# Optimization experiments

Measured on AMD Instinct MI355X. Metric: run time of the kernel, lower is better.

## Reference

```python
import jax, jax.numpy as jnp
import numpy as np

N_NODES = 100000
N_EDGES = 3200000
HID = 32
N_LAYERS = 3
EDGE_DIM = 2
NODE_IN = 2          # [P, Q]
V_DIM = 2            # [V_mag, V_angle]
VH = V_DIM + HID     # 34, per-node feature fed to the GNN layer
MSG_IN = 2 * VH + EDGE_DIM   # 70
UPD_IN = VH + HID            # 66


def setup_inputs() -> dict:
    key = jax.random.key(0)
    ks = jax.random.split(key, 16)
    s = lambda *sh: 1.0 / np.sqrt(sh[-2]) if len(sh) >= 2 else 0.0
    inp = {
        "P_Q_inj": jax.random.normal(ks[0], (N_NODES, NODE_IN), dtype=jnp.float32),
        "senders": jax.random.randint(ks[1], (N_EDGES,), 0, N_NODES, dtype=jnp.int32),
        "receivers": jax.random.randint(ks[2], (N_EDGES,), 0, N_NODES, dtype=jnp.int32),
        "edge_features": jax.random.normal(ks[3], (N_EDGES, EDGE_DIM), dtype=jnp.float32),
        "edge_mask": jax.random.uniform(ks[4], (N_EDGES,), dtype=jnp.float32),
        # input embedding Dense(hidden_dim)
        "W_in": jax.random.normal(ks[5], (NODE_IN, HID), dtype=jnp.float32) * s(NODE_IN, HID),
        "b_in": jnp.zeros((HID,), dtype=jnp.float32),
        # per-layer params (flax compact loop -> distinct params per layer), stacked on axis 0
        "W_msg": jax.random.normal(ks[6], (N_LAYERS, MSG_IN, HID), dtype=jnp.float32) * s(MSG_IN, HID),
        "b_msg": jnp.zeros((N_LAYERS, HID), dtype=jnp.float32),
        "W_upd": jax.random.normal(ks[7], (N_LAYERS, UPD_IN, HID), dtype=jnp.float32) * s(UPD_IN, HID),
        "b_upd": jnp.zeros((N_LAYERS, HID), dtype=jnp.float32),
        "W_delta": jax.random.normal(ks[8], (N_LAYERS, HID, V_DIM), dtype=jnp.float32) * s(HID, V_DIM),
        "b_delta": jnp.zeros((N_LAYERS, V_DIM), dtype=jnp.float32),
    }
    return inp


def _layer(v, senders, receivers, edge_features, edge_mask, W_msg, b_msg, W_upd, b_upd):
    # v: [N, VH] node features. Gather sender/receiver feats, edge-wise MLP message,
    # soft mask, scatter-sum to receivers, then dense node update.
    msg_in = jnp.concatenate([v[senders], v[receivers], edge_features], axis=-1)  # [E, 70]
    m = jax.nn.relu(msg_in @ W_msg + b_msg)                                       # [E, H]
    m = m * edge_mask[:, None]
    agg = jax.ops.segment_sum(m, receivers, num_segments=v.shape[0])              # [N, H]
    v_out = jnp.concatenate([v, agg], axis=-1) @ W_upd + b_upd                    # [N, H]
    return v_out


def reference(P_Q_inj, senders, receivers, edge_features, edge_mask,
              W_in, b_in, W_msg, b_msg, W_upd, b_upd, W_delta, b_delta):
    V_pred = jnp.zeros_like(P_Q_inj).at[:, 0].set(1.0)   # [N, 2]
    h = P_Q_inj @ W_in + b_in                            # [N, H]
    for l in range(N_LAYERS):
        v_input = jnp.concatenate([V_pred, h], axis=-1)  # [N, 34]
        v_out = _layer(v_input, senders, receivers, edge_features, edge_mask,
                       W_msg[l], b_msg[l], W_upd[l], b_upd[l])
        h = jax.nn.relu(v_out)
        delta_V = h @ W_delta[l] + b_delta[l]
        V_pred = V_pred + delta_V
    return V_pred
```

## Files before the change

kernel.cpp:

```cpp
#include <hip/hip_runtime.h>
#include <hip/hip_fp16.h>

#define NN 100000
#define NE 3200000
#define NB 1563
#define NBLK ((NN + 255) / 256)
#define CHUNK 8192
#define NCH 391
#define CAP 4096

typedef float f32x4 __attribute__((ext_vector_type(4)));
typedef unsigned int u32x4 __attribute__((ext_vector_type(4)));

__device__ __forceinline__ float2 h2f2(unsigned int u) {
  __half2 h;
  *reinterpret_cast<unsigned int*>(&h) = u;
  return __half22float2(h);
}
__device__ __forceinline__ unsigned int f2h2(float x, float y) {
  __half2 h = __floats2half2_rn(x, y);
  return *reinterpret_cast<unsigned int*>(&h);
}


__global__ __launch_bounds__(256) void k_hist(const int* __restrict__ recv, int* __restrict__ histmat) {
  __shared__ int h[NB];
  int t = threadIdx.x, c = blockIdx.x;
  for (int i = t; i < NB; i += 256) h[i] = 0;
  __syncthreads();
  int start = c * CHUNK;
  int end = min(start + CHUNK, NE);
  for (int i = start + t; i < end; i += 256)
    atomicAdd(&h[__builtin_nontemporal_load(recv + i) >> 6], 1);
  __syncthreads();
  for (int i = t; i < NB; i += 256) histmat[i * NCH + c] = h[i];
}


__global__ __launch_bounds__(64) void k_scanA(const int* __restrict__ histmat, int* __restrict__ total) {
  __shared__ int ps[64];
  int t = threadIdx.x, b = blockIdx.x;
  int s = 0;
  for (int c = t; c < NCH; c += 64) s += histmat[b * NCH + c];
  ps[t] = s;
  __syncthreads();
  for (int o = 32; o > 0; o >>= 1) {
    if (t < o) ps[t] += ps[t + o];
    __syncthreads();
  }
  if (t == 0) total[b] = ps[0];
}


__global__ __launch_bounds__(256) void k_scanB(const int* __restrict__ total, int* __restrict__ boff) {
  __shared__ int ps[256];
  int t = threadIdx.x;
  const int PER = (NB + 255) / 256;
  int v[PER];
  int s = 0;
#pragma unroll
  for (int k = 0; k < PER; k++) {
    int i = t * PER + k;
    v[k] = (i < NB) ? total[i] : 0;
    s += v[k];
  }
  ps[t] = s;
  __syncthreads();
  for (int o = 1; o < 256; o <<= 1) {
    int x = (t >= o) ? ps[t - o] : 0;
    __syncthreads();
    ps[t] += x;
    __syncthreads();
  }
  int run = (t > 0) ? ps[t - 1] : 0;
#pragma unroll
  for (int k = 0; k < PER; k++) {
    int i = t * PER + k;
    if (i < NB) {
      boff[i] = run;
      run += v[k];
    }
  }
  if (t == 255) boff[NB] = ps[255];
}


__global__ __launch_bounds__(64) void k_scanC(int* __restrict__ histmat, const int* __restrict__ boff) {
  __shared__ int ps[64];
  int t = threadIdx.x, b = blockIdx.x;
  const int PER = (NCH + 63) / 64;
  int v[PER];
  int s = 0;
#pragma unroll
  for (int k = 0; k < PER; k++) {
    int c = t * PER + k;
    v[k] = (c < NCH) ? histmat[b * NCH + c] : 0;
    s += v[k];
  }
  ps[t] = s;
  __syncthreads();
  for (int o = 1; o < 64; o <<= 1) {
    int x = (t >= o) ? ps[t - o] : 0;
    __syncthreads();
    ps[t] += x;
    __syncthreads();
  }
  int run = boff[b] + ((t > 0) ? ps[t - 1] : 0);
#pragma unroll
  for (int k = 0; k < PER; k++) {
    int c = t * PER + k;
    if (c < NCH) {
      histmat[b * NCH + c] = run;
      run += v[k];
    }
  }
}


__global__ __launch_bounds__(256) void k_scat(const int* __restrict__ send, const int* __restrict__ recv,
                                              const float2* __restrict__ ef, const float* __restrict__ mask,
                                              const int* __restrict__ boffc, float4* __restrict__ sorted) {
  __shared__ int lcnt[NB];
  int t = threadIdx.x, c = blockIdx.x;
  for (int i = t; i < NB; i += 256) lcnt[i] = 0;
  __syncthreads();
  int start = c * CHUNK;
  int end = min(start + CHUNK, NE);
  for (int i = start + t; i < end; i += 256) {
    int r = __builtin_nontemporal_load(recv + i);
    int s = __builtin_nontemporal_load(send + i);
    float2 e2 = ef[i];
    float mk = __builtin_nontemporal_load(mask + i);
    int b = r >> 6;
    int rank = atomicAdd(&lcnt[b], 1);
    int dst = boffc[b * NCH + c] + rank;
    float4 v;
    v.x = __int_as_float((s << 6) | (r & 63));
    v.y = e2.x;
    v.z = e2.y;
    v.w = mk;
    sorted[dst] = v;
  }
}


__global__ __launch_bounds__(256) void k_bsort(const int* __restrict__ boff, float4* __restrict__ sorted,
                                               int* __restrict__ row_off) {
  __shared__ int cnt[4096];
  __shared__ int part[256];
  __shared__ float4 stg[CAP];
  int t = threadIdx.x, b = blockIdx.x;
  int base = boff[b], end = boff[b + 1];
  int Eb = end - base;
  int n0 = b * 64;
  for (int i = t; i < 4096; i += 256) cnt[i] = 0;
  __syncthreads();
  for (int e = base + t; e < end; e += 256) {
    int pk = __float_as_int(sorted[e].x);
    int key = ((pk & 63) << 6) | (pk >> 17);
    atomicAdd(&cnt[key], 1);
  }
  __syncthreads();
  int s = 0;
#pragma unroll
  for (int k = 0; k < 16; k++) s += cnt[t * 16 + k];
  part[t] = s;
  __syncthreads();
  for (int o = 1; o < 256; o <<= 1) {
    int x = (t >= o) ? part[t - o] : 0;
    __syncthreads();
    part[t] += x;
    __syncthreads();
  }
  int run = part[t] - s;
#pragma unroll
  for (int k = 0; k < 16; k++) {
    int c = cnt[t * 16 + k];
    cnt[t * 16 + k] = run;
    run += c;
  }
  __syncthreads();
  if (t < 64) {
    int n = n0 + t;
    if (n < NN) row_off[n] = base + cnt[t << 6];
  }
  if (b == NB - 1 && t == 0) row_off[NN] = end;
  __syncthreads();
  for (int e = base + t; e < end; e += 256) {
    float4 r = sorted[e];
    int pk = __float_as_int(r.x);
    int key = ((pk & 63) << 6) | (pk >> 17);
    int p = atomicAdd(&cnt[key], 1);
    stg[p] = r;
  }
  __syncthreads();
  for (int i = t; i < Eb; i += 256) sorted[base + i] = stg[i];
}


__global__ __launch_bounds__(256) void k_init(const float2* __restrict__ PQ,
                                              const float* __restrict__ Win, const float* __restrict__ bin,
                                              const float* __restrict__ Wm, const float* __restrict__ bm,
                                              float* __restrict__ h, __half* __restrict__ a,
                                              float* __restrict__ bp, float2* __restrict__ Vp) {
  int n = blockIdx.x * 256 + threadIdx.x;
  if (n >= NN) return;
  float2 pq = PQ[n];
  float hh[32];
#pragma unroll
  for (int j = 0; j < 32; j++) hh[j] = fmaf(pq.x, Win[j], fmaf(pq.y, Win[32 + j], bin[j]));
  float4* h4 = (float4*)(h + (size_t)n * 32);
#pragma unroll
  for (int j = 0; j < 8; j++) h4[j] = make_float4(hh[4*j], hh[4*j+1], hh[4*j+2], hh[4*j+3]);
  Vp[n] = make_float2(1.0f, 0.0f);
  float av[32], bv[32];
#pragma unroll
  for (int j = 0; j < 32; j++) { av[j] = Wm[j]; bv[j] = Wm[34 * 32 + j] + bm[j]; }
#pragma unroll 1
  for (int k = 0; k < 32; k++) {
    float hk = hh[k];
#pragma unroll
    for (int j = 0; j < 32; j++) {
      av[j] = fmaf(hk, Wm[(2 + k) * 32 + j], av[j]);
      bv[j] = fmaf(hk, Wm[(36 + k) * 32 + j], bv[j]);
    }
  }
  u32x4* dst = (u32x4*)(a + (size_t)n * 32);
#pragma unroll
  for (int g = 0; g < 4; g++) {
    u32x4 p;
    p.x = f2h2(av[g*8+0], av[g*8+1]);
    p.y = f2h2(av[g*8+2], av[g*8+3]);
    p.z = f2h2(av[g*8+4], av[g*8+5]);
    p.w = f2h2(av[g*8+6], av[g*8+7]);
    dst[g] = p;
  }
  float4* b4 = (float4*)(bp + (size_t)n * 32);
#pragma unroll
  for (int j = 0; j < 8; j++) b4[j] = make_float4(bv[4*j], bv[4*j+1], bv[4*j+2], bv[4*j+3]);
}


__global__ __launch_bounds__(256) void k_edge(const __half* __restrict__ a, const float* __restrict__ bp,
                                              const int* __restrict__ row_off, const f32x4* __restrict__ sorted,
                                              const float* __restrict__ Wm, float* __restrict__ agg) {
  int t = threadIdx.x;
  int n = blockIdx.x * 64 + (t >> 2);
  if (n >= NN) return;
  int ch = (t & 3) * 8;
  const float* wr = Wm + 68 * 32 + ch;
  float w0[8], w1[8];
#pragma unroll
  for (int j = 0; j < 8; j++) { w0[j] = wr[j]; w1[j] = wr[32 + j]; }
  const float4 bna = *(const float4*)(bp + (size_t)n * 32 + ch);
  const float4 bnb = *(const float4*)(bp + (size_t)n * 32 + ch + 4);
  float bn[8] = {bna.x, bna.y, bna.z, bna.w, bnb.x, bnb.y, bnb.z, bnb.w};
  float acc[8] = {0.f, 0.f, 0.f, 0.f, 0.f, 0.f, 0.f, 0.f};
  int e0 = row_off[n], e1 = row_off[n + 1];
  f32x4 rec = {0.f, 0.f, 0.f, 0.f};
  if (e0 < e1) rec = __builtin_nontemporal_load(sorted + e0);
#pragma unroll 2
  for (int e = e0; e < e1; ++e) {
    int pk = __float_as_int(rec.x);
    float c0 = rec.y, c1 = rec.z, mk = rec.w;
    const u32x4 pa = *(const u32x4*)(a + (size_t)(pk >> 6) * 32 + ch);
    if (e + 1 < e1) rec = __builtin_nontemporal_load(sorted + e + 1);
    float2 f0 = h2f2(pa.x), f1 = h2f2(pa.y), f2 = h2f2(pa.z), f3 = h2f2(pa.w);
    float av[8] = {f0.x, f0.y, f1.x, f1.y, f2.x, f2.y, f3.x, f3.y};
#pragma unroll
    for (int j = 0; j < 8; j++)
      acc[j] = fmaf(fmaxf(av[j] + fmaf(c0, w0[j], fmaf(c1, w1[j], bn[j])), 0.f), mk, acc[j]);
  }
  float* gp = agg + (size_t)n * 32 + ch;
  *(float4*)gp       = make_float4(acc[0], acc[1], acc[2], acc[3]);
  *(float4*)(gp + 4) = make_float4(acc[4], acc[5], acc[6], acc[7]);
}


__global__ __launch_bounds__(256) void k_node(const float* __restrict__ agg,
                                              const float* __restrict__ Wu, const float* __restrict__ bu,
                                              const float* __restrict__ Wd, const float* __restrict__ bd,
                                              const float* __restrict__ Wm, const float* __restrict__ bm,
                                              float* __restrict__ h, __half* __restrict__ a,
                                              float* __restrict__ bp, float2* __restrict__ Vp,
                                              float2* __restrict__ out, int last) {
  int n = blockIdx.x * 256 + threadIdx.x;
  if (n >= NN) return;
  float2 vp = Vp[n];
  float v0 = vp.x, v1 = vp.y;
  float hh[32], ag[32];
  const float4* h4 = (const float4*)(h + (size_t)n * 32);
  const float4* g4 = (const float4*)(agg + (size_t)n * 32);
#pragma unroll
  for (int jj = 0; jj < 8; jj++) {
    float4 x = h4[jj];
    hh[4*jj] = x.x; hh[4*jj+1] = x.y; hh[4*jj+2] = x.z; hh[4*jj+3] = x.w;
    float4 y = g4[jj];
    ag[4*jj] = y.x; ag[4*jj+1] = y.y; ag[4*jj+2] = y.z; ag[4*jj+3] = y.w;
  }
  float vo[32];
#pragma unroll
  for (int j = 0; j < 32; j++) vo[j] = fmaf(v0, Wu[j], fmaf(v1, Wu[32 + j], bu[j]));
#pragma unroll 1
  for (int k = 0; k < 32; k++) {
    float hk = hh[k], ak = ag[k];
#pragma unroll
    for (int j = 0; j < 32; j++) {
      vo[j] = fmaf(hk, Wu[(2 + k) * 32 + j], vo[j]);
      vo[j] = fmaf(ak, Wu[(34 + k) * 32 + j], vo[j]);
    }
  }
#pragma unroll
  for (int j = 0; j < 32; j++) hh[j] = fmaxf(vo[j], 0.0f);
  float d0 = bd[0], d1 = bd[1];
#pragma unroll 1
  for (int k = 0; k < 32; k++) {
    d0 = fmaf(hh[k], Wd[2 * k], d0);
    d1 = fmaf(hh[k], Wd[2 * k + 1], d1);
  }
  v0 += d0;
  v1 += d1;
  if (last) {
    out[n] = make_float2(v0, v1);
    return;
  }
  Vp[n] = make_float2(v0, v1);
  float4* hw4 = (float4*)(h + (size_t)n * 32);
#pragma unroll
  for (int jj = 0; jj < 8; jj++) hw4[jj] = make_float4(hh[4*jj], hh[4*jj+1], hh[4*jj+2], hh[4*jj+3]);
  float av[32], bv[32];
#pragma unroll
  for (int j = 0; j < 32; j++) {
    av[j] = fmaf(v0, Wm[j], v1 * Wm[32 + j]);
    bv[j] = fmaf(v0, Wm[34 * 32 + j], fmaf(v1, Wm[35 * 32 + j], bm[j]));
  }
#pragma unroll 1
  for (int k = 0; k < 32; k++) {
    float hk = hh[k];
#pragma unroll
    for (int j = 0; j < 32; j++) {
      av[j] = fmaf(hk, Wm[(2 + k) * 32 + j], av[j]);
      bv[j] = fmaf(hk, Wm[(36 + k) * 32 + j], bv[j]);
    }
  }
  u32x4* dst = (u32x4*)(a + (size_t)n * 32);
#pragma unroll
  for (int g = 0; g < 4; g++) {
    u32x4 p;
    p.x = f2h2(av[g*8+0], av[g*8+1]);
    p.y = f2h2(av[g*8+2], av[g*8+3]);
    p.z = f2h2(av[g*8+4], av[g*8+5]);
    p.w = f2h2(av[g*8+6], av[g*8+7]);
    dst[g] = p;
  }
  float4* b4 = (float4*)(bp + (size_t)n * 32);
#pragma unroll
  for (int jj = 0; jj < 8; jj++) b4[jj] = make_float4(bv[4*jj], bv[4*jj+1], bv[4*jj+2], bv[4*jj+3]);
}


extern "C" void kernel_launch(void* const* d_in, const int* in_sizes, int n_in,
                              void* d_out, int out_size, void* d_ws, size_t ws_size,
                              hipStream_t stream) {
  const float* PQ   = (const float*)d_in[0];
  const int*   send = (const int*)d_in[1];
  const int*   recv = (const int*)d_in[2];
  const float* ef   = (const float*)d_in[3];
  const float* mask = (const float*)d_in[4];
  const float* Win  = (const float*)d_in[5];
  const float* bin  = (const float*)d_in[6];
  const float* Wmsg = (const float*)d_in[7];
  const float* bmsg = (const float*)d_in[8];
  const float* Wupd = (const float*)d_in[9];
  const float* bupd = (const float*)d_in[10];
  const float* Wdel = (const float*)d_in[11];
  const float* bdel = (const float*)d_in[12];
  float2* out = (float2*)d_out;

  char* w = (char*)d_ws;
  auto alloc = [&](size_t bytes) {
    char* p = w;
    w += (bytes + 255) & ~(size_t)255;
    return p;
  };
  float4* sorted = (float4*)alloc((size_t)NE * 16);
  int* histmat = (int*)alloc((size_t)NB * NCH * 4);
  int* total   = (int*)alloc((size_t)NB * 4);
  int* boff    = (int*)alloc(((size_t)NB + 1) * 4);
  int* row_off = (int*)alloc(((size_t)NN + 1) * 4);
  float* h    = (float*)alloc((size_t)NN * 32 * 4);
  __half* a   = (__half*)alloc((size_t)NN * 32 * 2);
  float* bp   = (float*)alloc((size_t)NN * 32 * 4);
  float* agg  = (float*)alloc((size_t)NN * 32 * 4);
  float2* Vp  = (float2*)alloc((size_t)NN * 8);

  k_hist<<<NCH, 256, 0, stream>>>(recv, histmat);
  k_scanA<<<NB, 64, 0, stream>>>(histmat, total);
  k_scanB<<<1, 256, 0, stream>>>(total, boff);
  k_scanC<<<NB, 64, 0, stream>>>(histmat, boff);
  k_scat<<<NCH, 256, 0, stream>>>(send, recv, (const float2*)ef, mask, histmat, sorted);
  k_bsort<<<NB, 256, 0, stream>>>(boff, sorted, row_off);

  k_init<<<NBLK, 256, 0, stream>>>((const float2*)PQ, Win, bin, Wmsg, bmsg, h, a, bp, Vp);

  for (int l = 0; l < 3; l++) {
    int last = (l == 2) ? 1 : 0;
    int lnext = (l + 1) % 3;
    k_edge<<<NB, 256, 0, stream>>>(a, bp, row_off, (const f32x4*)sorted, Wmsg + l * 70 * 32, agg);
    k_node<<<NBLK, 256, 0, stream>>>(agg, Wupd + l * 66 * 32, bupd + l * 32,
                                     Wdel + l * 64, bdel + l * 2,
                                     Wmsg + lnext * 70 * 32, bmsg + lnext * 32,
                                     h, a, bp, Vp, out, last);
  }
}
```

Before: 603.0 us.

## Restructure edge-sort preprocessing and deepen gather prefetch in edge kernel

Transposes the histogram matrix to chunk-major so the scan kernels become one thread per bucket with coalesced reads. k_scat now does a local counting sort of each chunk in shared memory before writing, so global writes into the sorted buffer are grouped by bucket. k_bsort keeps up to 8 records per thread in registers instead of staging them in a 64KB shared buffer, which frees LDS; this caps a bucket at 4096 edges (512 threads × 8) and silently drops any overflow. k_edge uses 512-thread blocks and prefetches the next edge's sender features one iteration ahead to hide gather latency.

Measured after the change: 658.2 us. +9.2%, slower.

```diff
diff --git a/kernel.cpp b/kernel.cpp
--- a/kernel.cpp
+++ b/kernel.cpp
@@ -7,7 +7,7 @@
 #define NBLK ((NN + 255) / 256)
 #define CHUNK 8192
 #define NCH 391
-#define CAP 4096
+#define NBE ((NN + 127) / 128)
 
 typedef float f32x4 __attribute__((ext_vector_type(4)));
 typedef unsigned int u32x4 __attribute__((ext_vector_type(4)));
@@ -23,32 +23,27 @@
 }
 
 
-__global__ __launch_bounds__(256) void k_hist(const int* __restrict__ recv, int* __restrict__ histmat) {
+__global__ __launch_bounds__(512) void k_hist(const int* __restrict__ recv, int* __restrict__ histmat) {
   __shared__ int h[NB];
   int t = threadIdx.x, c = blockIdx.x;
-  for (int i = t; i < NB; i += 256) h[i] = 0;
+  for (int i = t; i < NB; i += 512) h[i] = 0;
   __syncthreads();
   int start = c * CHUNK;
   int end = min(start + CHUNK, NE);
-  for (int i = start + t; i < end; i += 256)
+  for (int i = start + t; i < end; i += 512)
     atomicAdd(&h[__builtin_nontemporal_load(recv + i) >> 6], 1);
   __syncthreads();
-  for (int i = t; i < NB; i += 256) histmat[i * NCH + c] = h[i];
-}
-
-
-__global__ __launch_bounds__(64) void k_scanA(const int* __restrict__ histmat, int* __restrict__ total) {
-  __shared__ int ps[64];
-  int t = threadIdx.x, b = blockIdx.x;
+  for (int i = t; i < NB; i += 512) histmat[c * NB + i] = h[i];
+}
+
+
+__global__ __launch_bounds__(256) void k_scanA(const int* __restrict__ histmat, int* __restrict__ total) {
+  int b = blockIdx.x * 256 + threadIdx.x;
+  if (b >= NB) return;
   int s = 0;
-  for (int c = t; c < NCH; c += 64) s += histmat[b * NCH + c];
-  ps[t] = s;
-  __syncthreads();
-  for (int o = 32; o > 0; o >>= 1) {
-    if (t < o) ps[t] += ps[t + o];
-    __syncthreads();
-  }
-  if (t == 0) total[b] = ps[0];
+#pragma unroll 4
+  for (int c = 0; c < NCH; c++) s += histmat[c * NB + b];
+  total[b] = s;
 }
 
 
@@ -85,99 +80,135 @@
 }
 
 
-__global__ __launch_bounds__(64) void k_scanC(int* __restrict__ histmat, const int* __restrict__ boff) {
-  __shared__ int ps[64];
-  int t = threadIdx.x, b = blockIdx.x;
-  const int PER = (NCH + 63) / 64;
+__global__ __launch_bounds__(256) void k_scanC(int* __restrict__ histmat, const int* __restrict__ boff) {
+  int b = blockIdx.x * 256 + threadIdx.x;
+  if (b >= NB) return;
+  int run = boff[b];
+#pragma unroll 4
+  for (int c = 0; c < NCH; c++) {
+    int v = histmat[c * NB + b];
+    histmat[c * NB + b] = run;
+    run += v;
+  }
+}
+
+
+__global__ __launch_bounds__(512) void k_scat(const int* __restrict__ send, const int* __restrict__ recv,
+                                              const float2* __restrict__ ef, const float* __restrict__ mask,
+                                              const int* __restrict__ boffc, float4* __restrict__ sorted) {
+  __shared__ int lseg[NB];
+  __shared__ int cur[NB];
+  __shared__ int part[512];
+  __shared__ unsigned short inv[CHUNK];
+  int t = threadIdx.x, c = blockIdx.x;
+  for (int i = t; i < NB; i += 512) lseg[i] = 0;
+  __syncthreads();
+  int start = c * CHUNK;
+  int end = min(start + CHUNK, NE);
+  int len = end - start;
+  for (int i = start + t; i < end; i += 512)
+    atomicAdd(&lseg[__builtin_nontemporal_load(recv + i) >> 6], 1);
+  __syncthreads();
+  const int PER = (NB + 511) / 512;
   int v[PER];
   int s = 0;
 #pragma unroll
   for (int k = 0; k < PER; k++) {
-    int c = t * PER + k;
-    v[k] = (c < NCH) ? histmat[b * NCH + c] : 0;
+    int idx = t * PER + k;
+    v[k] = (idx < NB) ? lseg[idx] : 0;
     s += v[k];
   }
-  ps[t] = s;
-  __syncthreads();
-  for (int o = 1; o < 64; o <<= 1) {
-    int x = (t >= o) ? ps[t - o] : 0;
-    __syncthreads();
-    ps[t] += x;
-    __syncthreads();
-  }
-  int run = boff[b] + ((t > 0) ? ps[t - 1] : 0);
+  part[t] = s;
+  __syncthreads();
+  for (int o = 1; o < 512; o <<= 1) {
+    int x = (t >= o) ? part[t - o] : 0;
+    __syncthreads();
+    part[t] += x;
+    __syncthreads();
+  }
+  int run = (t > 0) ? part[t - 1] : 0;
 #pragma unroll
   for (int k = 0; k < PER; k++) {
-    int c = t * PER + k;
-    if (c < NCH) {
-      histmat[b * NCH + c] = run;
-      run += v[k];
+    int idx = t * PER + k;
+    if (idx < NB) {
+      int cc = v[k];
+      lseg[idx] = run;
+      cur[idx] = run;
+      run += cc;
     }
   }
-}
-
-
-__global__ __launch_bounds__(256) void k_scat(const int* __restrict__ send, const int* __restrict__ recv,
-                                              const float2* __restrict__ ef, const float* __restrict__ mask,
-                                              const int* __restrict__ boffc, float4* __restrict__ sorted) {
-  __shared__ int lcnt[NB];
-  int t = threadIdx.x, c = blockIdx.x;
-  for (int i = t; i < NB; i += 256) lcnt[i] = 0;
-  __syncthreads();
-  int start = c * CHUNK;
-  int end = min(start + CHUNK, NE);
-  for (int i = start + t; i < end; i += 256) {
-    int r = __builtin_nontemporal_load(recv + i);
-    int s = __builtin_nontemporal_load(send + i);
+  __syncthreads();
+  for (int i = start + t; i < end; i += 512) {
+    int b = recv[i] >> 6;
+    int p = atomicAdd(&cur[b], 1);
+    inv[p] = (unsigned short)(i - start);
+  }
+  __syncthreads();
+  const int* bo = boffc + c * NB;
+  for (int p = t; p < len; p += 512) {
+    int i = start + inv[p];
+    int r = recv[i];
+    int b = r >> 6;
+    int dst = bo[b] + (p - lseg[b]);
     float2 e2 = ef[i];
-    float mk = __builtin_nontemporal_load(mask + i);
-    int b = r >> 6;
-    int rank = atomicAdd(&lcnt[b], 1);
-    int dst = boffc[b * NCH + c] + rank;
-    float4 v;
-    v.x = __int_as_float((s << 6) | (r & 63));
-    v.y = e2.x;
-    v.z = e2.y;
-    v.w = mk;
-    sorted[dst] = v;
-  }
-}
-
-
-__global__ __launch_bounds__(256) void k_bsort(const int* __restrict__ boff, float4* __restrict__ sorted,
+    float4 vv;
+    vv.x = __int_as_float((send[i] << 6) | (r & 63));
+    vv.y = e2.x;
+    vv.z = e2.y;
+    vv.w = mask[i];
+    sorted[dst] = vv;
+  }
+}
+
+
+__global__ __launch_bounds__(512) void k_bsort(const int* __restrict__ boff, float4* __restrict__ sorted,
                                                int* __restrict__ row_off) {
   __shared__ int cnt[4096];
-  __shared__ int part[256];
-  __shared__ float4 stg[CAP];
+  __shared__ int part[512];
   int t = threadIdx.x, b = blockIdx.x;
   int base = boff[b], end = boff[b + 1];
-  int Eb = end - base;
   int n0 = b * 64;
-  for (int i = t; i < 4096; i += 256) cnt[i] = 0;
-  __syncthreads();
-  for (int e = base + t; e < end; e += 256) {
-    int pk = __float_as_int(sorted[e].x);
-    int key = ((pk & 63) << 6) | (pk >> 17);
-    atomicAdd(&cnt[key], 1);
-  }
-  __syncthreads();
+  for (int i = t; i < 4096; i += 512) cnt[i] = 0;
+  __syncthreads();
+  f32x4 r0, r1, r2, r3, r4, r5, r6, r7;
+  int key[8];
+  int nm = 0;
+#define LOADK(k, rk)                                        \
+  {                                                         \
+    int e = base + t + k * 512;                             \
+    if (e < end) {                                          \
+      rk = *(const f32x4*)(sorted + e);                     \
+      int pk = __float_as_int(rk.x);                        \
+      key[k] = ((pk & 63) << 6) | (pk >> 17);               \
+      atomicAdd(&cnt[key[k]], 1);                           \
+      nm = k + 1;                                           \
+    }                                                       \
+  }
+  LOADK(0, r0) LOADK(1, r1) LOADK(2, r2) LOADK(3, r3)
+  LOADK(4, r4) LOADK(5, r5) LOADK(6, r6) LOADK(7, r7)
+#undef LOADK
+  __syncthreads();
+  int vv[8];
   int s = 0;
 #pragma unroll
-  for (int k = 0; k < 16; k++) s += cnt[t * 16 + k];
+  for (int k = 0; k < 8; k++) {
+    vv[k] = cnt[t * 8 + k];
+    s += vv[k];
+  }
   part[t] = s;
   __syncthreads();
-  for (int o = 1; o < 256; o <<= 1) {
+  for (int o = 1; o < 512; o <<= 1) {
     int x = (t >= o) ? part[t - o] : 0;
     __syncthreads();
     part[t] += x;
     __syncthreads();
   }
-  int run = part[t] - s;
-#pragma unroll
-  for (int k = 0; k < 16; k++) {
-    int c = cnt[t * 16 + k];
-    cnt[t * 16 + k] = run;
-    run += c;
+  int run = (t > 0) ? part[t - 1] : 0;
+#pragma unroll
+  for (int k = 0; k < 8; k++) {
+    int cc = vv[k];
+    cnt[t * 8 + k] = run;
+    run += cc;
   }
   __syncthreads();
   if (t < 64) {
@@ -186,15 +217,14 @@
   }
   if (b == NB - 1 && t == 0) row_off[NN] = end;
   __syncthreads();
-  for (int e = base + t; e < end; e += 256) {
-    float4 r = sorted[e];
-    int pk = __float_as_int(r.x);
-    int key = ((pk & 63) << 6) | (pk >> 17);
-    int p = atomicAdd(&cnt[key], 1);
-    stg[p] = r;
-  }
-  __syncthreads();
-  for (int i = t; i < Eb; i += 256) sorted[base + i] = stg[i];
+#define STORK(k, rk)                                        \
+  if (k < nm) {                                             \
+    int p = atomicAdd(&cnt[key[k]], 1);                     \
+    *(f32x4*)(sorted + base + p) = rk;                      \
+  }
+  STORK(0, r0) STORK(1, r1) STORK(2, r2) STORK(3, r3)
+  STORK(4, r4) STORK(5, r5) STORK(6, r6) STORK(7, r7)
+#undef STORK
 }
 
 
@@ -241,11 +271,11 @@
 }
 
 
-__global__ __launch_bounds__(256) void k_edge(const __half* __restrict__ a, const float* __restrict__ bp,
+__global__ __launch_bounds__(512) void k_edge(const __half* __restrict__ a, const float* __restrict__ bp,
                                               const int* __restrict__ row_off, const f32x4* __restrict__ sorted,
                                               const float* __restrict__ Wm, float* __restrict__ agg) {
   int t = threadIdx.x;
-  int n = blockIdx.x * 64 + (t >> 2);
+  int n = blockIdx.x * 128 + (t >> 2);
   if (n >= NN) return;
   int ch = (t & 3) * 8;
   const float* wr = Wm + 68 * 32 + ch;
@@ -256,17 +286,22 @@
   const float4 bnb = *(const float4*)(bp + (size_t)n * 32 + ch + 4);
   float bn[8] = {bna.x, bna.y, bna.z, bna.w, bnb.x, bnb.y, bnb.z, bnb.w};
   float acc[8] = {0.f, 0.f, 0.f, 0.f, 0.f, 0.f, 0.f, 0.f};
+  const __half* abase = a + ch;
   int e0 = row_off[n], e1 = row_off[n + 1];
-  f32x4 rec = {0.f, 0.f, 0.f, 0.f};
-  if (e0 < e1) rec = __builtin_nontemporal_load(sorted + e0);
-#pragma unroll 2
+  f32x4 rec0 = {0.f, 0.f, 0.f, 0.f}, rec1 = {0.f, 0.f, 0.f, 0.f};
+  u32x4 pa0 = {0, 0, 0, 0};
+  if (e0 < e1) rec0 = __builtin_nontemporal_load(sorted + e0);
+  if (e0 + 1 < e1) rec1 = __builtin_nontemporal_load(sorted + e0 + 1);
+  if (e0 < e1) pa0 = *(const u32x4*)(abase + (size_t)(__float_as_int(rec0.x) >> 6) * 32);
   for (int e = e0; e < e1; ++e) {
-    int pk = __float_as_int(rec.x);
-    float c0 = rec.y, c1 = rec.z, mk = rec.w;
-    const u32x4 pa = *(const u32x4*)(a + (size_t)(pk >> 6) * 32 + ch);
-    if (e + 1 < e1) rec = __builtin_nontemporal_load(sorted + e + 1);
-    float2 f0 = h2f2(pa.x), f1 = h2f2(pa.y), f2 = h2f2(pa.z), f3 = h2f2(pa.w);
-    float av[8] = {f0.x, f0.y, f1.x, f1.y, f2.x, f2.y, f3.x, f3.y};
+    f32x4 rc = rec0;
+    u32x4 pa = pa0;
+    rec0 = rec1;
+    if (e + 2 < e1) rec1 = __builtin_nontemporal_load(sorted + e + 2);
+    if (e + 1 < e1) pa0 = *(const u32x4*)(abase + (size_t)(__float_as_int(rec0.x) >> 6) * 32);
+    float c0 = rc.y, c1 = rc.z, mk = rc.w;
+    float2 f0 = h2f2(pa.x), f1 = h2f2(pa.y), f2v = h2f2(pa.z), f3 = h2f2(pa.w);
+    float av[8] = {f0.x, f0.y, f1.x, f1.y, f2v.x, f2v.y, f3.x, f3.y};
 #pragma unroll
     for (int j = 0; j < 8; j++)
       acc[j] = fmaf(fmaxf(av[j] + fmaf(c0, w0[j], fmaf(c1, w1[j], bn[j])), 0.f), mk, acc[j]);
@@ -384,7 +419,7 @@
     return p;
   };
   float4* sorted = (float4*)alloc((size_t)NE * 16);
-  int* histmat = (int*)alloc((size_t)NB * NCH * 4);
+  int* histmat = (int*)alloc((size_t)NCH * NB * 4);
   int* total   = (int*)alloc((size_t)NB * 4);
   int* boff    = (int*)alloc(((size_t)NB + 1) * 4);
   int* row_off = (int*)alloc(((size_t)NN + 1) * 4);
@@ -394,19 +429,19 @@
   float* agg  = (float*)alloc((size_t)NN * 32 * 4);
   float2* Vp  = (float2*)alloc((size_t)NN * 8);
 
-  k_hist<<<NCH, 256, 0, stream>>>(recv, histmat);
-  k_scanA<<<NB, 64, 0, stream>>>(histmat, total);
+  k_hist<<<NCH, 512, 0, stream>>>(recv, histmat);
+  k_scanA<<<(NB + 255) / 256, 256, 0, stream>>>(histmat, total);
   k_scanB<<<1, 256, 0, stream>>>(total, boff);
-  k_scanC<<<NB, 64, 0, stream>>>(histmat, boff);
-  k_scat<<<NCH, 256, 0, stream>>>(send, recv, (const float2*)ef, mask, histmat, sorted);
-  k_bsort<<<NB, 256, 0, stream>>>(boff, sorted, row_off);
+  k_scanC<<<(NB + 255) / 256, 256, 0, stream>>>(histmat, boff);
+  k_scat<<<NCH, 512, 0, stream>>>(send, recv, (const float2*)ef, mask, histmat, sorted);
+  k_bsort<<<NB, 512, 0, stream>>>(boff, sorted, row_off);
 
   k_init<<<NBLK, 256, 0, stream>>>((const float2*)PQ, Win, bin, Wmsg, bmsg, h, a, bp, Vp);
 
   for (int l = 0; l < 3; l++) {
     int last = (l == 2) ? 1 : 0;
     int lnext = (l + 1) % 3;
-    k_edge<<<NB, 256, 0, stream>>>(a, bp, row_off, (const f32x4*)sorted, Wmsg + l * 70 * 32, agg);
+    k_edge<<<NBE, 512, 0, stream>>>(a, bp, row_off, (const f32x4*)sorted, Wmsg + l * 70 * 32, agg);
     k_node<<<NBLK, 256, 0, stream>>>(agg, Wupd + l * 66 * 32, bupd + l * 32,
                                      Wdel + l * 64, bdel + l * 2,
                                      Wmsg + lnext * 70 * 32, bmsg + lnext * 32,
```

## Stage bucket scatter in LDS and transpose histogram matrix for coalesced scans

Applied to the files above, without the earlier changes.

The scatter kernel now recounts its chunk's buckets, computes a block-local prefix scan, and stages the packed edge records in shared memory sorted by bucket. It then writes them to global memory in bucket-contiguous runs, replacing scattered 16-byte writes with mostly contiguous ones. The histogram matrix is transposed to chunk-major layout, so scanA and scanC become one-thread-per-bucket serial loops with coalesced accesses. Blocks grow to 1024 threads. The staging uses about 150KB of LDS per block, which limits occupancy, and the receiver histogram is computed a second time.

After: 577.6 us (median of 2 runs). -4.2%, faster.

```diff
diff --git a/kernel.cpp b/kernel.cpp
--- a/kernel.cpp
+++ b/kernel.cpp
@@ -23,32 +23,27 @@
 }
 
 
-__global__ __launch_bounds__(256) void k_hist(const int* __restrict__ recv, int* __restrict__ histmat) {
+__global__ __launch_bounds__(1024) void k_hist(const int* __restrict__ recv, int* __restrict__ histmat) {
   __shared__ int h[NB];
   int t = threadIdx.x, c = blockIdx.x;
-  for (int i = t; i < NB; i += 256) h[i] = 0;
+  for (int i = t; i < NB; i += 1024) h[i] = 0;
   __syncthreads();
   int start = c * CHUNK;
   int end = min(start + CHUNK, NE);
-  for (int i = start + t; i < end; i += 256)
+  for (int i = start + t; i < end; i += 1024)
     atomicAdd(&h[__builtin_nontemporal_load(recv + i) >> 6], 1);
   __syncthreads();
-  for (int i = t; i < NB; i += 256) histmat[i * NCH + c] = h[i];
-}
-
-
-__global__ __launch_bounds__(64) void k_scanA(const int* __restrict__ histmat, int* __restrict__ total) {
-  __shared__ int ps[64];
-  int t = threadIdx.x, b = blockIdx.x;
+  for (int i = t; i < NB; i += 1024) histmat[c * NB + i] = h[i];
+}
+
+
+__global__ __launch_bounds__(256) void k_scanA(const int* __restrict__ histmat, int* __restrict__ total) {
+  int b = blockIdx.x * 256 + threadIdx.x;
+  if (b >= NB) return;
   int s = 0;
-  for (int c = t; c < NCH; c += 64) s += histmat[b * NCH + c];
-  ps[t] = s;
-  __syncthreads();
-  for (int o = 32; o > 0; o >>= 1) {
-    if (t < o) ps[t] += ps[t + o];
-    __syncthreads();
-  }
-  if (t == 0) total[b] = ps[0];
+#pragma unroll 4
+  for (int c = 0; c < NCH; c++) s += histmat[c * NB + b];
+  total[b] = s;
 }
 
 
@@ -85,61 +80,83 @@
 }
 
 
-__global__ __launch_bounds__(64) void k_scanC(int* __restrict__ histmat, const int* __restrict__ boff) {
-  __shared__ int ps[64];
-  int t = threadIdx.x, b = blockIdx.x;
-  const int PER = (NCH + 63) / 64;
-  int v[PER];
-  int s = 0;
-#pragma unroll
-  for (int k = 0; k < PER; k++) {
-    int c = t * PER + k;
-    v[k] = (c < NCH) ? histmat[b * NCH + c] : 0;
-    s += v[k];
-  }
-  ps[t] = s;
-  __syncthreads();
-  for (int o = 1; o < 64; o <<= 1) {
-    int x = (t >= o) ? ps[t - o] : 0;
-    __syncthreads();
-    ps[t] += x;
-    __syncthreads();
-  }
-  int run = boff[b] + ((t > 0) ? ps[t - 1] : 0);
-#pragma unroll
-  for (int k = 0; k < PER; k++) {
-    int c = t * PER + k;
-    if (c < NCH) {
-      histmat[b * NCH + c] = run;
-      run += v[k];
-    }
-  }
-}
-
-
-__global__ __launch_bounds__(256) void k_scat(const int* __restrict__ send, const int* __restrict__ recv,
-                                              const float2* __restrict__ ef, const float* __restrict__ mask,
-                                              const int* __restrict__ boffc, float4* __restrict__ sorted) {
-  __shared__ int lcnt[NB];
+__global__ __launch_bounds__(256) void k_scanC(int* __restrict__ histmat, const int* __restrict__ boff) {
+  int b = blockIdx.x * 256 + threadIdx.x;
+  if (b >= NB) return;
+  int run = boff[b];
+#pragma unroll 4
+  for (int c = 0; c < NCH; c++) {
+    int v = histmat[c * NB + b];
+    histmat[c * NB + b] = run;
+    run += v;
+  }
+}
+
+
+__global__ __launch_bounds__(1024) void k_scat(const int* __restrict__ send, const int* __restrict__ recv,
+                                               const float2* __restrict__ ef, const float* __restrict__ mask,
+                                               const int* __restrict__ boffc, float4* __restrict__ sorted) {
+  __shared__ float4 stg[CHUNK];
+  __shared__ unsigned short bkt[CHUNK];
+  __shared__ int ofs[NB];
+  __shared__ int cur[NB];
+  __shared__ int wsum[16];
   int t = threadIdx.x, c = blockIdx.x;
-  for (int i = t; i < NB; i += 256) lcnt[i] = 0;
-  __syncthreads();
   int start = c * CHUNK;
   int end = min(start + CHUNK, NE);
-  for (int i = start + t; i < end; i += 256) {
-    int r = __builtin_nontemporal_load(recv + i);
-    int s = __builtin_nontemporal_load(send + i);
+  int len = end - start;
+  for (int i = t; i < NB; i += 1024) cur[i] = 0;
+  __syncthreads();
+  for (int i = start + t; i < end; i += 1024)
+    atomicAdd(&cur[__builtin_nontemporal_load(recv + i) >> 6], 1);
+  __syncthreads();
+  int v0 = (2 * t < NB) ? cur[2 * t] : 0;
+  int v1 = (2 * t + 1 < NB) ? cur[2 * t + 1] : 0;
+  int s = v0 + v1;
+  int lane = t & 63, wid = t >> 6;
+  for (int o = 1; o < 64; o <<= 1) {
+    int x = __shfl_up(s, o);
+    if (lane >= o) s += x;
+  }
+  if (lane == 63) wsum[wid] = s;
+  __syncthreads();
+  if (wid == 0) {
+    int ws = (lane < 16) ? wsum[lane] : 0;
+    for (int o = 1; o < 16; o <<= 1) {
+      int x = __shfl_up(ws, o);
+      if (lane >= o) ws += x;
+    }
+    if (lane < 16) wsum[lane] = ws;
+  }
+  __syncthreads();
+  int excl = s - v0 - v1 + ((wid > 0) ? wsum[wid - 1] : 0);
+  __syncthreads();
+  if (2 * t < NB) {
+    cur[2 * t] = excl;
+    ofs[2 * t] = boffc[c * NB + 2 * t] - excl;
+  }
+  if (2 * t + 1 < NB) {
+    cur[2 * t + 1] = excl + v0;
+    ofs[2 * t + 1] = boffc[c * NB + 2 * t + 1] - (excl + v0);
+  }
+  __syncthreads();
+  for (int i = start + t; i < end; i += 1024) {
+    int r = recv[i];
+    int b = r >> 6;
+    int p = atomicAdd(&cur[b], 1);
     float2 e2 = ef[i];
-    float mk = __builtin_nontemporal_load(mask + i);
-    int b = r >> 6;
-    int rank = atomicAdd(&lcnt[b], 1);
-    int dst = boffc[b * NCH + c] + rank;
-    float4 v;
-    v.x = __int_as_float((s << 6) | (r & 63));
-    v.y = e2.x;
-    v.z = e2.y;
-    v.w = mk;
-    sorted[dst] = v;
+    float4 vv;
+    vv.x = __int_as_float((send[i] << 6) | (r & 63));
+    vv.y = e2.x;
+    vv.z = e2.y;
+    vv.w = mask[i];
+    stg[p] = vv;
+    bkt[p] = (unsigned short)b;
+  }
+  __syncthreads();
+  for (int p = t; p < len; p += 1024) {
+    int b = bkt[p];
+    sorted[ofs[b] + p] = stg[p];
   }
 }
 
@@ -384,7 +401,7 @@
     return p;
   };
   float4* sorted = (float4*)alloc((size_t)NE * 16);
-  int* histmat = (int*)alloc((size_t)NB * NCH * 4);
+  int* histmat = (int*)alloc((size_t)NCH * NB * 4);
   int* total   = (int*)alloc((size_t)NB * 4);
   int* boff    = (int*)alloc(((size_t)NB + 1) * 4);
   int* row_off = (int*)alloc(((size_t)NN + 1) * 4);
@@ -394,11 +411,11 @@
   float* agg  = (float*)alloc((size_t)NN * 32 * 4);
   float2* Vp  = (float2*)alloc((size_t)NN * 8);
 
-  k_hist<<<NCH, 256, 0, stream>>>(recv, histmat);
-  k_scanA<<<NB, 64, 0, stream>>>(histmat, total);
+  k_hist<<<NCH, 1024, 0, stream>>>(recv, histmat);
+  k_scanA<<<(NB + 255) / 256, 256, 0, stream>>>(histmat, total);
   k_scanB<<<1, 256, 0, stream>>>(total, boff);
-  k_scanC<<<NB, 64, 0, stream>>>(histmat, boff);
-  k_scat<<<NCH, 256, 0, stream>>>(send, recv, (const float2*)ef, mask, histmat, sorted);
+  k_scanC<<<(NB + 255) / 256, 256, 0, stream>>>(histmat, boff);
+  k_scat<<<NCH, 1024, 0, stream>>>(send, recv, (const float2*)ef, mask, histmat, sorted);
   k_bsort<<<NB, 256, 0, stream>>>(boff, sorted, row_off);
 
   k_init<<<NBLK, 256, 0, stream>>>((const float2*)PQ, Win, bin, Wmsg, bmsg, h, a, bp, Vp);
```
